# Optimization experiments

Hardware: AMD Instinct MI355X
Metric: run time of the kernel (lower is better)

## Reference

```python
import jax, jax.numpy as jnp
import numpy as np
from functools import partial


def setup_inputs() -> dict:
    key = jax.random.key(0)
    ks = jax.random.split(key, 8)
    B, D, H, K, T = 256, 2048, 2048, 64, 32
    s = 1.0 / np.sqrt(H)  # PyTorch-style uniform init scale (use normal*s for simplicity)
    return {
        "x": jax.random.normal(ks[0], (B, D), dtype=jnp.float32),
        "eps": jax.random.normal(ks[1], (T, B, K), dtype=jnp.float32),
        "W_ih": jax.random.normal(ks[2], (4 * H, D), dtype=jnp.float32) * s,
        "W_hh": jax.random.normal(ks[3], (4 * H, H), dtype=jnp.float32) * s,
        "b_ih": jax.random.normal(ks[4], (4 * H,), dtype=jnp.float32) * s,
        "b_hh": jax.random.normal(ks[5], (4 * H,), dtype=jnp.float32) * s,
        "W_fe": jax.random.normal(ks[6], (2 * K, H), dtype=jnp.float32) * s,
        "b_fe": jax.random.normal(ks[7], (2 * K,), dtype=jnp.float32) * s,
        "num_ticks": T,
    }


def reference(x, eps, W_ih, W_hh, b_ih, b_hh, W_fe, b_fe, num_ticks):
    B = x.shape[0]
    H = W_hh.shape[1]
    K = eps.shape[-1]
    # x is fed unchanged every tick, so its gate contribution is precomputable.
    xg = x @ W_ih.T + b_ih + b_hh  # [B, 4H]

    def step(carry, e):
        h, c = carry
        g = xg + h @ W_hh.T  # [B, 4H]
        i, f, gg, o = jnp.split(g, 4, axis=-1)  # PyTorch LSTMCell gate order: i, f, g, o
        i = jax.nn.sigmoid(i)
        f = jax.nn.sigmoid(f)
        gg = jnp.tanh(gg)
        o = jax.nn.sigmoid(o)
        c = f * c + i * gg
        h = o * jnp.tanh(c)
        fe = h @ W_fe.T + b_fe  # [B, 2K]
        mus = fe[:, :K]
        sig = jax.nn.softplus(fe[:, K:] - 5.0)
        z = e * sig + mus
        return (h, c), (z, mus, sig)

    h0 = jnp.zeros((B, H), dtype=x.dtype)
    c0 = jnp.zeros((B, H), dtype=x.dtype)
    (h, c), (zs, mus, sigs) = jax.lax.scan(step, (h0, c0), eps)
    # torch stacks along dim=-1 -> [B, K, T]
    zs = jnp.moveaxis(zs, 0, -1)
    mus = jnp.moveaxis(mus, 0, -1)
    sigs = jnp.moveaxis(sigs, 0, -1)
    return zs, mus, sigs, (h, c)
```

## Files before the change

kernel.cpp:

```cpp
#include <hip/hip_runtime.h>
#include <math.h>


typedef short  short8  __attribute__((ext_vector_type(8)));
typedef float  floatx4 __attribute__((ext_vector_type(4)));

#define BB 256
#define HH 2048
#define G4 8192
#define KK 64
#define TT 32

__device__ __forceinline__ unsigned short f2bf(float f) {
  union { float f; unsigned int u; } v; v.f = f;
  unsigned int u = v.u;
  u += 0x7fffu + ((u >> 16) & 1u);
  return (unsigned short)(u >> 16);
}
__device__ __forceinline__ float sigmoidf_(float x) { return 1.0f / (1.0f + __expf(-x)); }
__device__ __forceinline__ float softplusf_(float x) {
  return (x > 20.0f) ? x : log1pf(__expf(x));
}
__device__ __forceinline__ short8 cvt8(const float* __restrict__ s) {
  float4 a = reinterpret_cast<const float4*>(s)[0];
  float4 b = reinterpret_cast<const float4*>(s)[1];
  short8 o;
  o[0] = f2bf(a.x); o[1] = f2bf(a.y); o[2] = f2bf(a.z); o[3] = f2bf(a.w);
  o[4] = f2bf(b.x); o[5] = f2bf(b.y); o[6] = f2bf(b.z); o[7] = f2bf(b.w);
  return o;
}

template <int PERM>
__global__ void cvt_w_kernel(const float* __restrict__ in,
                             unsigned short* __restrict__ out, int total) {
  int tid = blockIdx.x * 256 + threadIdx.x;
  if (tid >= total) return;
  int col = tid & 31;
  int k4  = (tid >> 5) & 63;
  int ph  = (tid >> 11) & 1;
  int blk = tid >> 12;
  int q = blk * 32 + col;
  int srcrow = PERM ? ((q & 3) * HH + (q >> 2)) : q;
  const float* src = in + (size_t)srcrow * HH + (ph * 128 + k4 * 2) * 8;
  short8 o0 = cvt8(src);
  short8 o1 = cvt8(src + 8);
  size_t ch = ((size_t)(blk * 2 + ph) * 128 + k4 * 2) * 32 + col;
  reinterpret_cast<short8*>(out)[ch]      = o0;
  reinterpret_cast<short8*>(out)[ch + 32] = o1;
}

__global__ void cvt_x_kernel(const float* __restrict__ in,
                             unsigned short* __restrict__ out) {
  int tid = blockIdx.x * 256 + threadIdx.x;
  int row = tid & 255, k8 = tid >> 8;
  short8 o = cvt8(in + (size_t)row * HH + k8 * 8);
  reinterpret_cast<short8*>(out)[tid] = o;
}

__device__ __forceinline__ void core_gemm(const short8* __restrict__ A8,
                                          const short8* __restrict__ Wg8,
                                          short8* L8, floatx4 acc[2][2]) {
  const int tid = threadIdx.x;
  const int lane = tid & 63, wave = tid >> 6;
  const int l15 = lane & 15, l4 = lane >> 4;
  const short8* Lr = L8 + l4 * 32 + l15;
  const int abase = l4 * 256 + wave * 32 + l15;
  for (int ph = 0; ph < 2; ++ph) {
    __syncthreads();
#pragma unroll
    for (int j = 0; j < 8; ++j)
      L8[tid + j * 512] = Wg8[ph * 4096 + tid + j * 512];
    __syncthreads();
    short8 Ar[4][2];
#pragma unroll
    for (int i = 0; i < 4; ++i) {
      Ar[i][0] = A8[abase +      (ph * 128 + i * 4) * 256];
      Ar[i][1] = A8[abase + 16 + (ph * 128 + i * 4) * 256];
    }
#pragma unroll
    for (int kt = 0; kt < 32; ++kt) {
      short8 a0 = Ar[kt & 3][0], a1 = Ar[kt & 3][1];
      if (kt < 28) {
        Ar[kt & 3][0] = A8[abase +      (ph * 128 + (kt + 4) * 4) * 256];
        Ar[kt & 3][1] = A8[abase + 16 + (ph * 128 + (kt + 4) * 4) * 256];
      }
      short8 b0 = Lr[kt * 128];
      short8 b1 = Lr[kt * 128 + 16];
      acc[0][0] = __builtin_amdgcn_mfma_f32_16x16x32_bf16(a0, b0, acc[0][0], 0, 0, 0);
      acc[0][1] = __builtin_amdgcn_mfma_f32_16x16x32_bf16(a0, b1, acc[0][1], 0, 0, 0);
      acc[1][0] = __builtin_amdgcn_mfma_f32_16x16x32_bf16(a1, b0, acc[1][0], 0, 0, 0);
      acc[1][1] = __builtin_amdgcn_mfma_f32_16x16x32_bf16(a1, b1, acc[1][1], 0, 0, 0);
    }
  }
}

__global__ __launch_bounds__(512, 2) void lstm_loop_kernel(
    unsigned short* __restrict__ HallT, const unsigned short* __restrict__ Wt2,
    const float* __restrict__ xg, float* __restrict__ outh,
    float* __restrict__ outc, unsigned int* __restrict__ bar) {
  __shared__ __align__(16) unsigned short Wlds[65536];
  const int tid = threadIdx.x;
  const int lane = tid & 63, wave = tid >> 6;
  const int l15 = lane & 15, l4 = lane >> 4;
  const int qb = blockIdx.x * 32, rw = wave * 32;
  const int gate = l15 & 3;
  const int base = lane & ~3;

  float xgr[2][2][4];
#pragma unroll
  for (int rt = 0; rt < 2; ++rt)
#pragma unroll
    for (int ct = 0; ct < 2; ++ct) {
      const int q = qb + ct * 16 + l15;
#pragma unroll
      for (int r = 0; r < 4; ++r) {
        const int row = rw + rt * 16 + l4 * 4 + r;
        xgr[rt][ct][r] = xg[(size_t)row * G4 + q];
      }
    }

  short8* L8 = reinterpret_cast<short8*>(Wlds);
  {
    const short8* Wg8 = reinterpret_cast<const short8*>(Wt2)
                        + (size_t)blockIdx.x * 8192;
#pragma unroll
    for (int j = 0; j < 16; ++j)
      L8[tid + j * 512] = Wg8[tid + j * 512];
  }
  __syncthreads();

  const short8* Lr = L8 + l4 * 32 + l15;
  const int abase = l4 * 256 + wave * 32 + l15;

  float creg[2][2][4];
#pragma unroll
  for (int rt = 0; rt < 2; ++rt)
#pragma unroll
    for (int ct = 0; ct < 2; ++ct)
#pragma unroll
      for (int r = 0; r < 4; ++r) creg[rt][ct][r] = 0.0f;

#pragma unroll 1
  for (int t = 0; t < TT; ++t) {
    unsigned short* Hout = HallT + (size_t)(t + 1) * 524288;

    floatx4 acc[2][2];
    floatx4 z4 = {0.f, 0.f, 0.f, 0.f};
    acc[0][0] = z4; acc[0][1] = z4; acc[1][0] = z4; acc[1][1] = z4;

    if (t > 0) {
      const short8* Ap = reinterpret_cast<const short8*>(HallT)
                         + (size_t)t * 65536 + abase;
      short8 Ar[12][2];
#pragma unroll
      for (int i = 0; i < 12; ++i) {
        Ar[i][0] = Ap[i * 1024];
        Ar[i][1] = Ap[i * 1024 + 16];
      }
      short8 Br[2][2];
      Br[0][0] = Lr[0];
      Br[0][1] = Lr[16];
#pragma unroll
      for (int kt = 0; kt < 64; ++kt) {
        short8 a0 = Ar[kt % 12][0], a1 = Ar[kt % 12][1];
        short8 b0 = Br[kt & 1][0],  b1 = Br[kt & 1][1];
        if (kt < 63) {
          Br[(kt + 1) & 1][0] = Lr[(kt + 1) * 128];
          Br[(kt + 1) & 1][1] = Lr[(kt + 1) * 128 + 16];
        }
        if (kt < 52) {
          Ar[kt % 12][0] = Ap[(kt + 12) * 1024];
          Ar[kt % 12][1] = Ap[(kt + 12) * 1024 + 16];
        }
        acc[0][0] = __builtin_amdgcn_mfma_f32_16x16x32_bf16(a0, b0, acc[0][0], 0, 0, 0);
        acc[0][1] = __builtin_amdgcn_mfma_f32_16x16x32_bf16(a0, b1, acc[0][1], 0, 0, 0);
        acc[1][0] = __builtin_amdgcn_mfma_f32_16x16x32_bf16(a1, b0, acc[1][0], 0, 0, 0);
        acc[1][1] = __builtin_amdgcn_mfma_f32_16x16x32_bf16(a1, b1, acc[1][1], 0, 0, 0);
      }
    }

    const int last = (t == TT - 1);
#pragma unroll
    for (int rt = 0; rt < 2; ++rt)
#pragma unroll
      for (int ct = 0; ct < 2; ++ct) {
        const floatx4 av = acc[rt][ct];
        const int q = qb + ct * 16 + l15;
        const int u = q >> 2;
#pragma unroll
        for (int r = 0; r < 4; ++r) {
          const int row = rw + rt * 16 + l4 * 4 + r;
          float g = av[r] + xgr[rt][ct][r];
          float act = (gate == 2) ? tanhf(g) : sigmoidf_(g);
          float iv = __shfl(act, base);
          float fv = __shfl(act, base + 1);
          float gv = __shfl(act, base + 2);
          float ov = __shfl(act, base + 3);
          if (gate == 0) {
            float cnew = fv * creg[rt][ct][r] + iv * gv;
            float hnew = ov * tanhf(cnew);
            creg[rt][ct][r] = cnew;
            Hout[(size_t)(blockIdx.x * 256 + row) * 8 + (u & 7)] = f2bf(hnew);
            if (last) {
              const size_t ci = (size_t)row * HH + u;
              outh[ci] = hnew; outc[ci] = cnew;
            }
          }
        }
      }

    if (t < TT - 1) {
      __syncthreads();
      if (tid == 0) {
        __hip_atomic_fetch_add(bar, 1u, __ATOMIC_RELEASE,
                               __HIP_MEMORY_SCOPE_AGENT);
        const unsigned int target = (unsigned int)(t + 1) * 256u;
        while (__hip_atomic_load(bar, __ATOMIC_ACQUIRE,
                                 __HIP_MEMORY_SCOPE_AGENT) < target)
          __builtin_amdgcn_s_sleep(2);
      }
      __syncthreads();
    }
  }
}

__global__ __launch_bounds__(512) void xg_kernel(
    const unsigned short* __restrict__ XT, const unsigned short* __restrict__ Wih,
    const float* __restrict__ b_ih, const float* __restrict__ b_hh,
    float* __restrict__ xg) {
  __shared__ __align__(16) unsigned short Wlds[32768];
  floatx4 acc[2][2];
  floatx4 z4 = {0.f, 0.f, 0.f, 0.f};
  acc[0][0] = z4; acc[0][1] = z4; acc[1][0] = z4; acc[1][1] = z4;
  core_gemm(reinterpret_cast<const short8*>(XT),
            reinterpret_cast<const short8*>(Wih) + (size_t)blockIdx.x * 8192,
            reinterpret_cast<short8*>(Wlds), acc);

  const int tid = threadIdx.x, lane = tid & 63, wave = tid >> 6;
  const int l15 = lane & 15, l4 = lane >> 4;
  const int qb = blockIdx.x * 32, rw = wave * 32;
#pragma unroll
  for (int rt = 0; rt < 2; ++rt)
#pragma unroll
    for (int ct = 0; ct < 2; ++ct) {
      const int q = qb + ct * 16 + l15;
      const float bias = b_ih[(q & 3) * HH + (q >> 2)] + b_hh[(q & 3) * HH + (q >> 2)];
#pragma unroll
      for (int r = 0; r < 4; ++r) {
        const int row = rw + rt * 16 + l4 * 4 + r;
        xg[(size_t)row * G4 + q] = acc[rt][ct][r] + bias;
      }
    }
}

__global__ __launch_bounds__(512) void fe_kernel(
    const unsigned short* __restrict__ HallT, const unsigned short* __restrict__ Wfe,
    const float* __restrict__ b_fe, float* __restrict__ fe) {
  const int t = blockIdx.x >> 2, cg_ = blockIdx.x & 3;
  __shared__ __align__(16) unsigned short Wlds[32768];
  floatx4 acc[2][2];
  floatx4 z4 = {0.f, 0.f, 0.f, 0.f};
  acc[0][0] = z4; acc[0][1] = z4; acc[1][0] = z4; acc[1][1] = z4;
  core_gemm(reinterpret_cast<const short8*>(HallT) + (size_t)(t + 1) * 65536,
            reinterpret_cast<const short8*>(Wfe) + (size_t)cg_ * 8192,
            reinterpret_cast<short8*>(Wlds), acc);

  const int tid = threadIdx.x, lane = tid & 63, wave = tid >> 6;
  const int l15 = lane & 15, l4 = lane >> 4;
  const int rw = wave * 32;
#pragma unroll
  for (int rt = 0; rt < 2; ++rt)
#pragma unroll
    for (int ct = 0; ct < 2; ++ct) {
      const int col = cg_ * 32 + ct * 16 + l15;
      const float bias = b_fe[col];
#pragma unroll
      for (int r = 0; r < 4; ++r) {
        const int row = rw + rt * 16 + l4 * 4 + r;
        fe[((size_t)t * 256 + row) * 128 + col] = acc[rt][ct][r] + bias;
      }
    }
}

__global__ void z_kernel(const float* __restrict__ eps, const float* __restrict__ fe,
                         float* __restrict__ out) {
  const int tid = blockIdx.x * blockDim.x + threadIdx.x;
  const int tt = tid >> 14;
  const int b = (tid >> 6) & 255;
  const int k = tid & 63;
  const int frow = tt * 256 + b;
  const float mus = fe[frow * 128 + k];
  const float sig = softplusf_(fe[frow * 128 + 64 + k] - 5.0f);
  const float z = eps[tid] * sig + mus;
  const int o = (b * KK + k) * TT + tt;
  out[o] = z;
  out[524288 + o] = mus;
  out[2 * 524288 + o] = sig;
}

extern "C" void kernel_launch(void* const* d_in, const int* in_sizes, int n_in,
                              void* d_out, int out_size, void* d_ws, size_t ws_size,
                              hipStream_t stream) {
  const float* x    = (const float*)d_in[0];
  const float* eps  = (const float*)d_in[1];
  const float* W_ih = (const float*)d_in[2];
  const float* W_hh = (const float*)d_in[3];
  const float* b_ih = (const float*)d_in[4];
  const float* b_hh = (const float*)d_in[5];
  const float* W_fe = (const float*)d_in[6];
  const float* b_fe = (const float*)d_in[7];
  float* out = (float*)d_out;

  const size_t BH  = (size_t)BB * HH;
  const size_t BKT = (size_t)BB * KK * TT;

  char* p = (char*)d_ws;
  auto nxt = [&](size_t bytes) -> char* {
    char* r = p; p += (bytes + 255) & ~(size_t)255; return r;
  };
  unsigned short* Wbig  = (unsigned short*)nxt((size_t)G4 * HH * 2);
  float*          xg    = (float*)nxt((size_t)BB * G4 * 4);
  unsigned short* HallT = (unsigned short*)nxt((size_t)(TT + 1) * BH * 2);
  unsigned short* XT    = (unsigned short*)nxt(BH * 2);
  unsigned short* Wfeb  = (unsigned short*)nxt((size_t)128 * HH * 2);
  float*          fe    = (float*)nxt((size_t)(TT * BB) * 128 * 4);
  unsigned int*   bar   = (unsigned int*)nxt(256);

  hipMemsetAsync(bar, 0, 256, stream);

  cvt_x_kernel<<<256, 256, 0, stream>>>(x, XT);
  cvt_w_kernel<0><<<64, 256, 0, stream>>>(W_fe, Wfeb, 16384);
  cvt_w_kernel<1><<<4096, 256, 0, stream>>>(W_ih, Wbig, 1048576);
  xg_kernel<<<256, 512, 0, stream>>>(XT, Wbig, b_ih, b_hh, xg);
  cvt_w_kernel<1><<<4096, 256, 0, stream>>>(W_hh, Wbig, 1048576);

  lstm_loop_kernel<<<256, 512, 0, stream>>>(
      HallT, Wbig, xg, out + 3 * BKT, out + 3 * BKT + BH, bar);

  fe_kernel<<<128, 512, 0, stream>>>(HallT, Wfeb, b_fe, fe);
  z_kernel<<<2048, 256, 0, stream>>>(eps, fe, out);
}
```

Baseline: 1.284 ms.

## Double threads per block in persistent LSTM loop, halving per-wave tile

The recurrent loop kernel now launches 1024 threads (16 waves) per block instead of 512. Each wave computes a 16-row by 32-column gate tile with two MFMA accumulators instead of 32x32 with four. This spreads the per-step matmul over more waves to cut per-wave serial latency in the latency-bound recurrence. In exchange, each wave issues more global loads of the hidden state relative to its compute (A fragments are no longer reused across two B tiles). The 1024-thread bound also leaves fewer registers per thread, and the prefetch depth and B double-buffering were reduced.

```diff
diff --git a/kernel.cpp b/kernel.cpp
--- a/kernel.cpp
+++ b/kernel.cpp
@@ -94,7 +94,7 @@
   }
 }
 
-__global__ __launch_bounds__(512, 2) void lstm_loop_kernel(
+__global__ __launch_bounds__(1024) void lstm_loop_kernel(
     unsigned short* __restrict__ HallT, const unsigned short* __restrict__ Wt2,
     const float* __restrict__ xg, float* __restrict__ outh,
     float* __restrict__ outc, unsigned int* __restrict__ bar) {
@@ -102,112 +102,92 @@
   const int tid = threadIdx.x;
   const int lane = tid & 63, wave = tid >> 6;
   const int l15 = lane & 15, l4 = lane >> 4;
-  const int qb = blockIdx.x * 32, rw = wave * 32;
+  const int qb = blockIdx.x * 32, rw = wave * 16;
   const int gate = l15 & 3;
   const int base = lane & ~3;
 
-  float xgr[2][2][4];
-#pragma unroll
-  for (int rt = 0; rt < 2; ++rt)
-#pragma unroll
-    for (int ct = 0; ct < 2; ++ct) {
-      const int q = qb + ct * 16 + l15;
-#pragma unroll
-      for (int r = 0; r < 4; ++r) {
-        const int row = rw + rt * 16 + l4 * 4 + r;
-        xgr[rt][ct][r] = xg[(size_t)row * G4 + q];
-      }
-    }
+  float xgr[2][4];
+#pragma unroll
+  for (int ct = 0; ct < 2; ++ct) {
+    const int q = qb + ct * 16 + l15;
+#pragma unroll
+    for (int r = 0; r < 4; ++r) {
+      const int row = rw + l4 * 4 + r;
+      xgr[ct][r] = xg[(size_t)row * G4 + q];
+    }
+  }
 
   short8* L8 = reinterpret_cast<short8*>(Wlds);
   {
     const short8* Wg8 = reinterpret_cast<const short8*>(Wt2)
                         + (size_t)blockIdx.x * 8192;
 #pragma unroll
-    for (int j = 0; j < 16; ++j)
-      L8[tid + j * 512] = Wg8[tid + j * 512];
+    for (int j = 0; j < 8; ++j)
+      L8[tid + j * 1024] = Wg8[tid + j * 1024];
   }
   __syncthreads();
 
   const short8* Lr = L8 + l4 * 32 + l15;
-  const int abase = l4 * 256 + wave * 32 + l15;
-
-  float creg[2][2][4];
-#pragma unroll
-  for (int rt = 0; rt < 2; ++rt)
-#pragma unroll
-    for (int ct = 0; ct < 2; ++ct)
-#pragma unroll
-      for (int r = 0; r < 4; ++r) creg[rt][ct][r] = 0.0f;
+  const int abase = l4 * 256 + wave * 16 + l15;
+
+  float creg[2][4];
+#pragma unroll
+  for (int ct = 0; ct < 2; ++ct)
+#pragma unroll
+    for (int r = 0; r < 4; ++r) creg[ct][r] = 0.0f;
 
 #pragma unroll 1
   for (int t = 0; t < TT; ++t) {
     unsigned short* Hout = HallT + (size_t)(t + 1) * 524288;
 
-    floatx4 acc[2][2];
+    floatx4 acc[2];
     floatx4 z4 = {0.f, 0.f, 0.f, 0.f};
-    acc[0][0] = z4; acc[0][1] = z4; acc[1][0] = z4; acc[1][1] = z4;
+    acc[0] = z4; acc[1] = z4;
 
     if (t > 0) {
       const short8* Ap = reinterpret_cast<const short8*>(HallT)
                          + (size_t)t * 65536 + abase;
-      short8 Ar[12][2];
-#pragma unroll
-      for (int i = 0; i < 12; ++i) {
-        Ar[i][0] = Ap[i * 1024];
-        Ar[i][1] = Ap[i * 1024 + 16];
-      }
-      short8 Br[2][2];
-      Br[0][0] = Lr[0];
-      Br[0][1] = Lr[16];
+      short8 Ar[8];
+#pragma unroll
+      for (int i = 0; i < 8; ++i) Ar[i] = Ap[i * 1024];
 #pragma unroll
       for (int kt = 0; kt < 64; ++kt) {
-        short8 a0 = Ar[kt % 12][0], a1 = Ar[kt % 12][1];
-        short8 b0 = Br[kt & 1][0],  b1 = Br[kt & 1][1];
-        if (kt < 63) {
-          Br[(kt + 1) & 1][0] = Lr[(kt + 1) * 128];
-          Br[(kt + 1) & 1][1] = Lr[(kt + 1) * 128 + 16];
-        }
-        if (kt < 52) {
-          Ar[kt % 12][0] = Ap[(kt + 12) * 1024];
-          Ar[kt % 12][1] = Ap[(kt + 12) * 1024 + 16];
-        }
-        acc[0][0] = __builtin_amdgcn_mfma_f32_16x16x32_bf16(a0, b0, acc[0][0], 0, 0, 0);
-        acc[0][1] = __builtin_amdgcn_mfma_f32_16x16x32_bf16(a0, b1, acc[0][1], 0, 0, 0);
-        acc[1][0] = __builtin_amdgcn_mfma_f32_16x16x32_bf16(a1, b0, acc[1][0], 0, 0, 0);
-        acc[1][1] = __builtin_amdgcn_mfma_f32_16x16x32_bf16(a1, b1, acc[1][1], 0, 0, 0);
+        short8 a0 = Ar[kt & 7];
+        if (kt < 56) Ar[kt & 7] = Ap[(kt + 8) * 1024];
+        short8 b0 = Lr[kt * 128];
+        short8 b1 = Lr[kt * 128 + 16];
+        acc[0] = __builtin_amdgcn_mfma_f32_16x16x32_bf16(a0, b0, acc[0], 0, 0, 0);
+        acc[1] = __builtin_amdgcn_mfma_f32_16x16x32_bf16(a0, b1, acc[1], 0, 0, 0);
       }
     }
 
     const int last = (t == TT - 1);
 #pragma unroll
-    for (int rt = 0; rt < 2; ++rt)
-#pragma unroll
-      for (int ct = 0; ct < 2; ++ct) {
-        const floatx4 av = acc[rt][ct];
-        const int q = qb + ct * 16 + l15;
-        const int u = q >> 2;
-#pragma unroll
-        for (int r = 0; r < 4; ++r) {
-          const int row = rw + rt * 16 + l4 * 4 + r;
-          float g = av[r] + xgr[rt][ct][r];
-          float act = (gate == 2) ? tanhf(g) : sigmoidf_(g);
-          float iv = __shfl(act, base);
-          float fv = __shfl(act, base + 1);
-          float gv = __shfl(act, base + 2);
-          float ov = __shfl(act, base + 3);
-          if (gate == 0) {
-            float cnew = fv * creg[rt][ct][r] + iv * gv;
-            float hnew = ov * tanhf(cnew);
-            creg[rt][ct][r] = cnew;
-            Hout[(size_t)(blockIdx.x * 256 + row) * 8 + (u & 7)] = f2bf(hnew);
-            if (last) {
-              const size_t ci = (size_t)row * HH + u;
-              outh[ci] = hnew; outc[ci] = cnew;
-            }
+    for (int ct = 0; ct < 2; ++ct) {
+      const floatx4 av = acc[ct];
+      const int q = qb + ct * 16 + l15;
+      const int u = q >> 2;
+#pragma unroll
+      for (int r = 0; r < 4; ++r) {
+        const int row = rw + l4 * 4 + r;
+        float g = av[r] + xgr[ct][r];
+        float act = (gate == 2) ? tanhf(g) : sigmoidf_(g);
+        float iv = __shfl(act, base);
+        float fv = __shfl(act, base + 1);
+        float gv = __shfl(act, base + 2);
+        float ov = __shfl(act, base + 3);
+        if (gate == 0) {
+          float cnew = fv * creg[ct][r] + iv * gv;
+          float hnew = ov * tanhf(cnew);
+          creg[ct][r] = cnew;
+          Hout[(size_t)(blockIdx.x * 256 + row) * 8 + (u & 7)] = f2bf(hnew);
+          if (last) {
+            const size_t ci = (size_t)row * HH + u;
+            outh[ci] = hnew; outc[ci] = cnew;
           }
         }
       }
+    }
 
     if (t < TT - 1) {
       __syncthreads();
@@ -334,7 +314,7 @@
   xg_kernel<<<256, 512, 0, stream>>>(XT, Wbig, b_ih, b_hh, xg);
   cvt_w_kernel<1><<<4096, 256, 0, stream>>>(W_hh, Wbig, 1048576);
 
-  lstm_loop_kernel<<<256, 512, 0, stream>>>(
+  lstm_loop_kernel<<<256, 1024, 0, stream>>>(
       HallT, Wbig, xg, out + 3 * BKT, out + 3 * BKT + BH, bar);
 
   fe_kernel<<<128, 512, 0, stream>>>(HallT, Wfeb, b_fe, fe);
```

Result: faster. 1.045 ms (-18.6%).
